# Performance work log

Measured on AMD Instinct MI355X. Metric: run time of the kernel, lower is better.

The kernel has to match this reference:

```python
import jax, jax.numpy as jnp
import numpy as np

N = 62          # EEG channels (nodes per graph)
B = 512         # graphs in batch
K = 2           # SGConv propagation steps
F_IN = 128
H = 64
C = 3


def _complete_graph_edge_index():
    # edge e = g*N*N + i*N + j connects node g*N+i -> g*N+j,
    # matching edge_weight = Wsym.reshape(-1).repeat(B) ordering.
    base = np.arange(N)
    ii = np.tile(np.repeat(base, N), B)
    jj = np.tile(np.tile(base, N), B)
    off = np.repeat(np.arange(B) * N, N * N)
    return jnp.asarray(np.stack([off + ii, off + jj]).astype(np.int32))


def setup_inputs() -> dict:
    key = jax.random.key(0)
    ks = jax.random.split(key, 6)
    n_total = B * N
    x = jax.random.normal(ks[0], (n_total, F_IN), dtype=jnp.float32)
    edge_weight_tril = jax.random.normal(ks[1], (N * (N + 1) // 2,), dtype=jnp.float32)
    W1 = jax.random.normal(ks[2], (H, F_IN), dtype=jnp.float32) * (1.0 / np.sqrt(F_IN))
    b1 = jax.random.normal(ks[3], (H,), dtype=jnp.float32) * 0.01
    W2 = jax.random.normal(ks[4], (C, H), dtype=jnp.float32) * (1.0 / np.sqrt(H))
    b2 = jax.random.normal(ks[5], (C,), dtype=jnp.float32) * 0.01
    edge_index = _complete_graph_edge_index()
    batch = jnp.asarray(np.repeat(np.arange(B), N).astype(np.int32))
    return {"x": x, "edge_weight_tril": edge_weight_tril, "W1": W1, "b1": b1,
            "W2": W2, "b2": b2, "edge_index": edge_index, "batch": batch,
            "batch_size": B}


def reference(x, edge_weight_tril, W1, b1, W2, b2, edge_index, batch, batch_size):
    n_total = x.shape[0]
    # rebuild symmetric dense adjacency from lower-tri params
    xs, ys = np.tril_indices(N)
    Wm = jnp.zeros((N, N), dtype=x.dtype).at[xs, ys].set(edge_weight_tril)
    Wsym = Wm + Wm.T - jnp.diag(jnp.diag(Wm))
    ew = jnp.tile(Wsym.reshape(-1), batch_size)            # [B*N*N]

    row, col = edge_index[0], edge_index[1]
    # symmetric normalization (graph already contains self loops)
    deg = jax.ops.segment_sum(jnp.abs(ew), row, num_segments=n_total)
    dinv = jnp.where(deg > 0, deg ** -0.5, 0.0)
    norm = dinv[row] * ew * dinv[col]                      # [E]

    # K-step SGConv propagation: gather, scale, scatter-add
    h = x
    for _ in range(K):
        h = jax.ops.segment_sum(norm[:, None] * h[row], col, num_segments=n_total)

    h = jax.nn.relu(h @ W1.T + b1)                         # [n_total, H]
    pooled = jax.ops.segment_sum(h, batch, num_segments=batch_size)  # global_add_pool
    latent_v = pooled                                      # dropout in eval mode = identity
    logits = latent_v @ W2.T + b2
    logp = jax.nn.log_softmax(logits, axis=-1)
    return latent_v, logp
```

## Files before the change

### kernel.cpp

```cpp
#include <hip/hip_runtime.h>
#include <math.h>

#define NN  62
#define BGR 512
#define FIN 128
#define HD  64
#define NC  3

typedef __attribute__((ext_vector_type(8))) short          bf16x8;
typedef __attribute__((ext_vector_type(4))) float          f32x4;
typedef __attribute__((ext_vector_type(4))) unsigned short us4;

static __device__ __forceinline__ unsigned short f2bf(float f) {
    union { float f; unsigned u; } v; v.f = f;
    unsigned u = v.u;
    return (unsigned short)((u + 0x7fffu + ((u >> 16) & 1u)) >> 16);
}
static __device__ __forceinline__ float bf2f(unsigned short h) {
    union { unsigned u; float f; } v; v.u = ((unsigned)h) << 16;
    return v.f;
}


__global__ __launch_bounds__(256) void precomp(
    const float* __restrict__ tril, const float* __restrict__ W1,
    unsigned short* __restrict__ ws) {
    __shared__ unsigned short AH[9216];
    __shared__ float dinvS[64];

    const int t = threadIdx.x;
    const int lane = t & 63, wv = t >> 6, quad = lane >> 4, l15 = lane & 15;

    {
        const float4* w14 = (const float4*)W1;
        for (int e = t; e < 2048; e += 256) {
            int h = e >> 5, f4 = e & 31;
            float4 v = w14[e];
            us4 hh, ll;
            hh[0] = f2bf(v.x); ll[0] = f2bf(v.x - bf2f(hh[0]));
            hh[1] = f2bf(v.y); ll[1] = f2bf(v.y - bf2f(hh[1]));
            hh[2] = f2bf(v.z); ll[2] = f2bf(v.z - bf2f(hh[2]));
            hh[3] = f2bf(v.w); ll[3] = f2bf(v.w - bf2f(hh[3]));
            *(us4*)&ws[ 8192 + h * 136 + f4 * 4] = hh;
            *(us4*)&ws[16896 + h * 136 + f4 * 4] = ll;
        }
    }

    if (t < 64) {
        float s = 0.f;
        if (t < NN) {
            for (int j = 0; j < NN; ++j) {
                int hi = max(t, j), lo = min(t, j);
                s += fabsf(tril[hi * (hi + 1) / 2 + lo]);
            }
            s = (s > 0.f) ? (1.0f / sqrtf(s)) : 0.f;
        }
        dinvS[t] = s;
    }
    __syncthreads();

    for (int e4 = t; e4 < 1024; e4 += 256) {
        int i = e4 >> 4, j0 = (e4 & 15) * 4;
        float di = dinvS[i];
        float4 dj4 = *(float4*)&dinvS[j0];
        float dja[4] = {dj4.x, dj4.y, dj4.z, dj4.w};
        us4 hh, ll;
#pragma unroll
        for (int r = 0; r < 4; ++r) {
            int j = j0 + r;
            float w = 0.f;
            if (i < NN && j < NN) {
                int hi = max(i, j), lo = min(i, j);
                w = tril[hi * (hi + 1) / 2 + lo];
            }
            float v = di * w * dja[r];
            hh[r] = f2bf(v);
            ll[r] = f2bf(v - bf2f(hh[r]));
        }
        *(us4*)&AH[       i * 72 + j0] = hh;
        *(us4*)&AH[4608 + i * 72 + j0] = ll;
    }
    __syncthreads();

    f32x4 za0 = {0,0,0,0}, za1 = {0,0,0,0}, za2 = {0,0,0,0}, za3 = {0,0,0,0};
    {
        const int arow = (16 * wv + l15) * 72 + quad * 8;
#pragma unroll
        for (int c = 0; c < 2; ++c) {
            bf16x8 ahi = *(bf16x8*)&AH[arow + c * 32];
            bf16x8 alo = *(bf16x8*)&AH[4608 + arow + c * 32];
#define ATILE(ACC, NT) { \
            int bo = (16 * NT + l15) * 72 + quad * 8 + c * 32; \
            bf16x8 bhi = *(bf16x8*)&AH[bo]; \
            bf16x8 blo = *(bf16x8*)&AH[4608 + bo]; \
            ACC = __builtin_amdgcn_mfma_f32_16x16x32_bf16(ahi, bhi, ACC, 0, 0, 0); \
            ACC = __builtin_amdgcn_mfma_f32_16x16x32_bf16(ahi, blo, ACC, 0, 0, 0); \
            ACC = __builtin_amdgcn_mfma_f32_16x16x32_bf16(alo, bhi, ACC, 0, 0, 0); \
            ACC = __builtin_amdgcn_mfma_f32_16x16x32_bf16(alo, blo, ACC, 0, 0, 0); }
            ATILE(za0, 0) ATILE(za1, 1) ATILE(za2, 2) ATILE(za3, 3)
#undef ATILE
        }
    }

    {
        const int mbase = 16 * wv + quad * 4;
#define A2W(ACC, NT) { \
        int n = 16 * NT + l15; \
        us4 hh, ll; \
        hh[0] = f2bf(ACC[0]); ll[0] = f2bf(ACC[0] - bf2f(hh[0])); \
        hh[1] = f2bf(ACC[1]); ll[1] = f2bf(ACC[1] - bf2f(hh[1])); \
        hh[2] = f2bf(ACC[2]); ll[2] = f2bf(ACC[2] - bf2f(hh[2])); \
        hh[3] = f2bf(ACC[3]); ll[3] = f2bf(ACC[3] - bf2f(hh[3])); \
        *(us4*)&ws[       n * 64 + mbase] = hh; \
        *(us4*)&ws[4096 + n * 64 + mbase] = ll; }
        A2W(za0, 0) A2W(za1, 1) A2W(za2, 2) A2W(za3, 3)
#undef A2W
    }
}

__global__ __launch_bounds__(256) void gcn_all(
    const float* __restrict__ x, const float* __restrict__ b1,
    const float* __restrict__ W2, const float* __restrict__ b2,
    const unsigned short* __restrict__ ws, float* __restrict__ out) {
    __shared__ unsigned short SH[34816];
    __shared__ float TAIL[1088 + 64];
    float* partial = TAIL;
    float* b1S     = TAIL + 1088;

    const int t = threadIdx.x;
    const int g = blockIdx.x;
    const int lane = t & 63, wv = t >> 6, quad = lane >> 4, l15 = lane & 15;

    if (t < 16) *(float4*)&b1S[4 * t] = ((const float4*)b1)[t];

    const int a2off = (16 * wv + l15) * 64 + quad * 8;
    bf16x8 A2h0 = *(const bf16x8*)&ws[a2off];
    bf16x8 A2l0 = *(const bf16x8*)&ws[4096 + a2off];
    bf16x8 A2h1 = *(const bf16x8*)&ws[a2off + 32];
    bf16x8 A2l1 = *(const bf16x8*)&ws[4096 + a2off + 32];

    const float4* xg4 = (const float4*)(x + (size_t)g * NN * FIN);
    for (int e = t; e < 2048; e += 256) {
        int row = e >> 5, k4 = e & 31;
        float4 v = {0.f, 0.f, 0.f, 0.f};
        if (e < 1984) v = xg4[e];
        us4 hh, ll;
        hh[0] = f2bf(v.x); ll[0] = f2bf(v.x - bf2f(hh[0]));
        hh[1] = f2bf(v.y); ll[1] = f2bf(v.y - bf2f(hh[1]));
        hh[2] = f2bf(v.z); ll[2] = f2bf(v.z - bf2f(hh[2]));
        hh[3] = f2bf(v.w); ll[3] = f2bf(v.w - bf2f(hh[3]));
        *(us4*)&SH[       row * 136 + k4 * 4] = hh;
        *(us4*)&SH[8704 + row * 136 + k4 * 4] = ll;
    }
    {
        const uint4* src = (const uint4*)(ws + 8192);
        uint4* dst = (uint4*)(SH + 17408);
        for (int i = t; i < 2176; i += 256) dst[i] = src[i];
    }
    __syncthreads();

    f32x4 y0 = {0,0,0,0}, y1 = {0,0,0,0}, y2 = {0,0,0,0}, y3 = {0,0,0,0};
    {
        const int arow = (16 * wv + l15) * 136 + quad * 8;
#pragma unroll
        for (int c = 0; c < 4; ++c) {
            bf16x8 ahi = *(bf16x8*)&SH[arow + c * 32];
            bf16x8 alo = *(bf16x8*)&SH[8704 + arow + c * 32];
#define P1TILE(ACC, NT) { \
            int bo = (16 * NT + l15) * 136 + quad * 8 + c * 32; \
            bf16x8 bhi = *(bf16x8*)&SH[17408 + bo]; \
            bf16x8 blo = *(bf16x8*)&SH[26112 + bo]; \
            ACC = __builtin_amdgcn_mfma_f32_16x16x32_bf16(ahi, bhi, ACC, 0, 0, 0); \
            ACC = __builtin_amdgcn_mfma_f32_16x16x32_bf16(ahi, blo, ACC, 0, 0, 0); \
            ACC = __builtin_amdgcn_mfma_f32_16x16x32_bf16(alo, bhi, ACC, 0, 0, 0); \
            ACC = __builtin_amdgcn_mfma_f32_16x16x32_bf16(alo, blo, ACC, 0, 0, 0); }
            P1TILE(y0, 0) P1TILE(y1, 1) P1TILE(y2, 2) P1TILE(y3, 3)
#undef P1TILE
        }
    }
    __syncthreads();

    {
        const int mbase = 16 * wv + quad * 4;
#define SPLITW(ACC, NT) { \
        int n = 16 * NT + l15; \
        us4 hh, ll; \
        hh[0] = f2bf(ACC[0]); ll[0] = f2bf(ACC[0] - bf2f(hh[0])); \
        hh[1] = f2bf(ACC[1]); ll[1] = f2bf(ACC[1] - bf2f(hh[1])); \
        hh[2] = f2bf(ACC[2]); ll[2] = f2bf(ACC[2] - bf2f(hh[2])); \
        hh[3] = f2bf(ACC[3]); ll[3] = f2bf(ACC[3] - bf2f(hh[3])); \
        *(us4*)&SH[       n * 72 + mbase] = hh; \
        *(us4*)&SH[4608 + n * 72 + mbase] = ll; }
        SPLITW(y0, 0) SPLITW(y1, 1) SPLITW(y2, 2) SPLITW(y3, 3)
#undef SPLITW
    }
    __syncthreads();

    f32x4 z0 = {0,0,0,0}, z1 = {0,0,0,0}, z2 = {0,0,0,0}, z3 = {0,0,0,0};
    {
#define P2TILE(ACC, NT, AH_, AL_, CO) { \
        int bo = (16 * NT + l15) * 72 + quad * 8 + CO; \
        bf16x8 bhi = *(bf16x8*)&SH[bo]; \
        bf16x8 blo = *(bf16x8*)&SH[4608 + bo]; \
        ACC = __builtin_amdgcn_mfma_f32_16x16x32_bf16(AH_, bhi, ACC, 0, 0, 0); \
        ACC = __builtin_amdgcn_mfma_f32_16x16x32_bf16(AH_, blo, ACC, 0, 0, 0); \
        ACC = __builtin_amdgcn_mfma_f32_16x16x32_bf16(AL_, bhi, ACC, 0, 0, 0); \
        ACC = __builtin_amdgcn_mfma_f32_16x16x32_bf16(AL_, blo, ACC, 0, 0, 0); }
        P2TILE(z0, 0, A2h0, A2l0, 0) P2TILE(z1, 1, A2h0, A2l0, 0)
        P2TILE(z2, 2, A2h0, A2l0, 0) P2TILE(z3, 3, A2h0, A2l0, 0)
        P2TILE(z0, 0, A2h1, A2l1, 32) P2TILE(z1, 1, A2h1, A2l1, 32)
        P2TILE(z2, 2, A2h1, A2l1, 32) P2TILE(z3, 3, A2h1, A2l1, 32)
#undef P2TILE
    }

    {
        const int mbase = 16 * wv + quad * 4;
        const int slot = 4 * wv + quad;
#define POOL(ACC, NT) { \
        int n = 16 * NT + l15; \
        float bn = b1S[n]; \
        float p = 0.f; \
        if (mbase + 0 < 62) p += fmaxf(ACC[0] + bn, 0.f); \
        if (mbase + 1 < 62) p += fmaxf(ACC[1] + bn, 0.f); \
        if (mbase + 2 < 62) p += fmaxf(ACC[2] + bn, 0.f); \
        if (mbase + 3 < 62) p += fmaxf(ACC[3] + bn, 0.f); \
        partial[n * 17 + slot] = p; }
        POOL(z0, 0) POOL(z1, 1) POOL(z2, 2) POOL(z3, 3)
#undef POOL
    }
    __syncthreads();

    if (t < HD) {
        float s = 0.f;
#pragma unroll
        for (int q = 0; q < 16; ++q) s += partial[t * 17 + q];
        out[(size_t)g * HD + t] = s;
        float l0 = s * W2[t];
        float l1 = s * W2[64 + t];
        float l2 = s * W2[128 + t];
#pragma unroll
        for (int off = 32; off > 0; off >>= 1) {
            l0 += __shfl_down(l0, off);
            l1 += __shfl_down(l1, off);
            l2 += __shfl_down(l2, off);
        }
        if (t == 0) {
            l0 += b2[0]; l1 += b2[1]; l2 += b2[2];
            float m = fmaxf(l0, fmaxf(l1, l2));
            float lse = m + logf(expf(l0 - m) + expf(l1 - m) + expf(l2 - m));
            float* lp = out + (size_t)BGR * HD + (size_t)g * NC;
            lp[0] = l0 - lse; lp[1] = l1 - lse; lp[2] = l2 - lse;
        }
    }
}

extern "C" void kernel_launch(void* const* d_in, const int* in_sizes, int n_in,
                              void* d_out, int out_size, void* d_ws, size_t ws_size,
                              hipStream_t stream) {
    const float* x    = (const float*)d_in[0];
    const float* tril = (const float*)d_in[1];
    const float* W1   = (const float*)d_in[2];
    const float* b1   = (const float*)d_in[3];
    const float* W2   = (const float*)d_in[4];
    const float* b2   = (const float*)d_in[5];
    float* out = (float*)d_out;
    unsigned short* ws = (unsigned short*)d_ws;

    precomp<<<1, 256, 0, stream>>>(tril, W1, ws);
    gcn_all<<<BGR, 256, 0, stream>>>(x, b1, W2, b2, ws, out);
}
```

Baseline: 105.1 us.

## Fuse adjacency precompute into main kernel and drop lo*lo split-bf16 MFMA terms

Removes the single-block precomp launch. Every block now recomputes dinv, the normalized A, A^2 and the bf16 hi/lo split of W1 itself, and reads x rows straight into registers instead of staging them in LDS. It also drops the lo*lo MFMA term in all three matmuls, cutting MFMA count by a quarter at a small precision cost. The trade is redundant per-block A^2 and W1 conversion work and heavier register use, in exchange for removing the serial launch dependency and the LDS staging of x.

```diff
diff --git a/kernel.cpp b/kernel.cpp
--- a/kernel.cpp
+++ b/kernel.cpp
@@ -21,28 +21,44 @@
     return v.f;
 }
 
-
-__global__ __launch_bounds__(256) void precomp(
-    const float* __restrict__ tril, const float* __restrict__ W1,
-    unsigned short* __restrict__ ws) {
-    __shared__ unsigned short AH[9216];
-    __shared__ float dinvS[64];
+__global__ __launch_bounds__(256) void gcn_all(
+    const float* __restrict__ x, const float* __restrict__ tril,
+    const float* __restrict__ W1, const float* __restrict__ b1,
+    const float* __restrict__ W2, const float* __restrict__ b2,
+    float* __restrict__ out) {
+    __shared__ unsigned short SH[35840];
+    __shared__ float TAIL[1088 + 64 + 64];
+    float* partial = TAIL;
+    float* b1S     = TAIL + 1088;
+    float* dinvS   = TAIL + 1152;
 
     const int t = threadIdx.x;
+    const int g = blockIdx.x;
     const int lane = t & 63, wv = t >> 6, quad = lane >> 4, l15 = lane & 15;
 
-    {
-        const float4* w14 = (const float4*)W1;
-        for (int e = t; e < 2048; e += 256) {
-            int h = e >> 5, f4 = e & 31;
-            float4 v = w14[e];
-            us4 hh, ll;
-            hh[0] = f2bf(v.x); ll[0] = f2bf(v.x - bf2f(hh[0]));
-            hh[1] = f2bf(v.y); ll[1] = f2bf(v.y - bf2f(hh[1]));
-            hh[2] = f2bf(v.z); ll[2] = f2bf(v.z - bf2f(hh[2]));
-            hh[3] = f2bf(v.w); ll[3] = f2bf(v.w - bf2f(hh[3]));
-            *(us4*)&ws[ 8192 + h * 136 + f4 * 4] = hh;
-            *(us4*)&ws[16896 + h * 136 + f4 * 4] = ll;
+    if (t < 16) *(float4*)&b1S[4 * t] = ((const float4*)b1)[t];
+
+    bf16x8 xh[4], xl[4];
+    {
+        const int xr = 16 * wv + l15;
+        if (xr < NN) {
+            const float* xrow = x + (size_t)g * NN * FIN + (size_t)xr * FIN + quad * 8;
+#pragma unroll
+            for (int c = 0; c < 4; ++c) {
+                float4 a = *(const float4*)(xrow + c * 32);
+                float4 b = *(const float4*)(xrow + c * 32 + 4);
+                float vv[8] = {a.x, a.y, a.z, a.w, b.x, b.y, b.z, b.w};
+#pragma unroll
+                for (int k = 0; k < 8; ++k) {
+                    unsigned short h = f2bf(vv[k]);
+                    xh[c][k] = (short)h;
+                    xl[c][k] = (short)f2bf(vv[k] - bf2f(h));
+                }
+            }
+        } else {
+            bf16x8 zv = {0, 0, 0, 0, 0, 0, 0, 0};
+#pragma unroll
+            for (int c = 0; c < 4; ++c) { xh[c] = zv; xl[c] = zv; }
         }
     }
 
@@ -77,140 +93,99 @@
             hh[r] = f2bf(v);
             ll[r] = f2bf(v - bf2f(hh[r]));
         }
-        *(us4*)&AH[       i * 72 + j0] = hh;
-        *(us4*)&AH[4608 + i * 72 + j0] = ll;
+        *(us4*)&SH[17408 + i * 72 + j0] = hh;
+        *(us4*)&SH[22016 + i * 72 + j0] = ll;
+    }
+    {
+        const float4* w14 = (const float4*)W1;
+        for (int e = t; e < 2048; e += 256) {
+            int h = e >> 5, f4 = e & 31;
+            float4 v = w14[e];
+            us4 hh, ll;
+            hh[0] = f2bf(v.x); ll[0] = f2bf(v.x - bf2f(hh[0]));
+            hh[1] = f2bf(v.y); ll[1] = f2bf(v.y - bf2f(hh[1]));
+            hh[2] = f2bf(v.z); ll[2] = f2bf(v.z - bf2f(hh[2]));
+            hh[3] = f2bf(v.w); ll[3] = f2bf(v.w - bf2f(hh[3]));
+            *(us4*)&SH[       h * 136 + f4 * 4] = hh;
+            *(us4*)&SH[8704 + h * 136 + f4 * 4] = ll;
+        }
     }
     __syncthreads();
 
     f32x4 za0 = {0,0,0,0}, za1 = {0,0,0,0}, za2 = {0,0,0,0}, za3 = {0,0,0,0};
     {
-        const int arow = (16 * wv + l15) * 72 + quad * 8;
+        const int arow = 17408 + (16 * wv + l15) * 72 + quad * 8;
 #pragma unroll
         for (int c = 0; c < 2; ++c) {
-            bf16x8 ahi = *(bf16x8*)&AH[arow + c * 32];
-            bf16x8 alo = *(bf16x8*)&AH[4608 + arow + c * 32];
+            bf16x8 ahi = *(bf16x8*)&SH[arow + c * 32];
+            bf16x8 alo = *(bf16x8*)&SH[4608 + arow + c * 32];
 #define ATILE(ACC, NT) { \
-            int bo = (16 * NT + l15) * 72 + quad * 8 + c * 32; \
-            bf16x8 bhi = *(bf16x8*)&AH[bo]; \
-            bf16x8 blo = *(bf16x8*)&AH[4608 + bo]; \
+            int bo = 17408 + (16 * NT + l15) * 72 + quad * 8 + c * 32; \
+            bf16x8 bhi = *(bf16x8*)&SH[bo]; \
+            bf16x8 blo = *(bf16x8*)&SH[4608 + bo]; \
             ACC = __builtin_amdgcn_mfma_f32_16x16x32_bf16(ahi, bhi, ACC, 0, 0, 0); \
             ACC = __builtin_amdgcn_mfma_f32_16x16x32_bf16(ahi, blo, ACC, 0, 0, 0); \
-            ACC = __builtin_amdgcn_mfma_f32_16x16x32_bf16(alo, bhi, ACC, 0, 0, 0); \
-            ACC = __builtin_amdgcn_mfma_f32_16x16x32_bf16(alo, blo, ACC, 0, 0, 0); }
+            ACC = __builtin_amdgcn_mfma_f32_16x16x32_bf16(alo, bhi, ACC, 0, 0, 0); }
             ATILE(za0, 0) ATILE(za1, 1) ATILE(za2, 2) ATILE(za3, 3)
 #undef ATILE
         }
     }
 
+    f32x4 y0 = {0,0,0,0}, y1 = {0,0,0,0}, y2 = {0,0,0,0}, y3 = {0,0,0,0};
+    {
+#pragma unroll
+        for (int c = 0; c < 4; ++c) {
+            bf16x8 ahi = xh[c];
+            bf16x8 alo = xl[c];
+#define P1TILE(ACC, NT) { \
+            int bo = (16 * NT + l15) * 136 + quad * 8 + c * 32; \
+            bf16x8 bhi = *(bf16x8*)&SH[bo]; \
+            bf16x8 blo = *(bf16x8*)&SH[8704 + bo]; \
+            ACC = __builtin_amdgcn_mfma_f32_16x16x32_bf16(ahi, bhi, ACC, 0, 0, 0); \
+            ACC = __builtin_amdgcn_mfma_f32_16x16x32_bf16(ahi, blo, ACC, 0, 0, 0); \
+            ACC = __builtin_amdgcn_mfma_f32_16x16x32_bf16(alo, bhi, ACC, 0, 0, 0); }
+            P1TILE(y0, 0) P1TILE(y1, 1) P1TILE(y2, 2) P1TILE(y3, 3)
+#undef P1TILE
+        }
+    }
+    __syncthreads();
+
     {
         const int mbase = 16 * wv + quad * 4;
-#define A2W(ACC, NT) { \
+#define SPLITW(ACC, NT, HIOFF, LOOFF) { \
         int n = 16 * NT + l15; \
         us4 hh, ll; \
         hh[0] = f2bf(ACC[0]); ll[0] = f2bf(ACC[0] - bf2f(hh[0])); \
         hh[1] = f2bf(ACC[1]); ll[1] = f2bf(ACC[1] - bf2f(hh[1])); \
         hh[2] = f2bf(ACC[2]); ll[2] = f2bf(ACC[2] - bf2f(hh[2])); \
         hh[3] = f2bf(ACC[3]); ll[3] = f2bf(ACC[3] - bf2f(hh[3])); \
-        *(us4*)&ws[       n * 64 + mbase] = hh; \
-        *(us4*)&ws[4096 + n * 64 + mbase] = ll; }
-        A2W(za0, 0) A2W(za1, 1) A2W(za2, 2) A2W(za3, 3)
-#undef A2W
-    }
-}
-
-__global__ __launch_bounds__(256) void gcn_all(
-    const float* __restrict__ x, const float* __restrict__ b1,
-    const float* __restrict__ W2, const float* __restrict__ b2,
-    const unsigned short* __restrict__ ws, float* __restrict__ out) {
-    __shared__ unsigned short SH[34816];
-    __shared__ float TAIL[1088 + 64];
-    float* partial = TAIL;
-    float* b1S     = TAIL + 1088;
-
-    const int t = threadIdx.x;
-    const int g = blockIdx.x;
-    const int lane = t & 63, wv = t >> 6, quad = lane >> 4, l15 = lane & 15;
-
-    if (t < 16) *(float4*)&b1S[4 * t] = ((const float4*)b1)[t];
-
-    const int a2off = (16 * wv + l15) * 64 + quad * 8;
-    bf16x8 A2h0 = *(const bf16x8*)&ws[a2off];
-    bf16x8 A2l0 = *(const bf16x8*)&ws[4096 + a2off];
-    bf16x8 A2h1 = *(const bf16x8*)&ws[a2off + 32];
-    bf16x8 A2l1 = *(const bf16x8*)&ws[4096 + a2off + 32];
-
-    const float4* xg4 = (const float4*)(x + (size_t)g * NN * FIN);
-    for (int e = t; e < 2048; e += 256) {
-        int row = e >> 5, k4 = e & 31;
-        float4 v = {0.f, 0.f, 0.f, 0.f};
-        if (e < 1984) v = xg4[e];
-        us4 hh, ll;
-        hh[0] = f2bf(v.x); ll[0] = f2bf(v.x - bf2f(hh[0]));
-        hh[1] = f2bf(v.y); ll[1] = f2bf(v.y - bf2f(hh[1]));
-        hh[2] = f2bf(v.z); ll[2] = f2bf(v.z - bf2f(hh[2]));
-        hh[3] = f2bf(v.w); ll[3] = f2bf(v.w - bf2f(hh[3]));
-        *(us4*)&SH[       row * 136 + k4 * 4] = hh;
-        *(us4*)&SH[8704 + row * 136 + k4 * 4] = ll;
-    }
-    {
-        const uint4* src = (const uint4*)(ws + 8192);
-        uint4* dst = (uint4*)(SH + 17408);
-        for (int i = t; i < 2176; i += 256) dst[i] = src[i];
-    }
-    __syncthreads();
-
-    f32x4 y0 = {0,0,0,0}, y1 = {0,0,0,0}, y2 = {0,0,0,0}, y3 = {0,0,0,0};
-    {
-        const int arow = (16 * wv + l15) * 136 + quad * 8;
-#pragma unroll
-        for (int c = 0; c < 4; ++c) {
+        *(us4*)&SH[(HIOFF) + n * 72 + mbase] = hh; \
+        *(us4*)&SH[(LOOFF) + n * 72 + mbase] = ll; }
+        SPLITW(y0, 0, 26624, 31232) SPLITW(y1, 1, 26624, 31232)
+        SPLITW(y2, 2, 26624, 31232) SPLITW(y3, 3, 26624, 31232)
+        SPLITW(za0, 0, 17408, 22016) SPLITW(za1, 1, 17408, 22016)
+        SPLITW(za2, 2, 17408, 22016) SPLITW(za3, 3, 17408, 22016)
+#undef SPLITW
+    }
+    __syncthreads();
+
+    f32x4 z0 = {0,0,0,0}, z1 = {0,0,0,0}, z2 = {0,0,0,0}, z3 = {0,0,0,0};
+    {
+        const int arow = 17408 + (16 * wv + l15) * 72 + quad * 8;
+#pragma unroll
+        for (int c = 0; c < 2; ++c) {
             bf16x8 ahi = *(bf16x8*)&SH[arow + c * 32];
-            bf16x8 alo = *(bf16x8*)&SH[8704 + arow + c * 32];
-#define P1TILE(ACC, NT) { \
-            int bo = (16 * NT + l15) * 136 + quad * 8 + c * 32; \
-            bf16x8 bhi = *(bf16x8*)&SH[17408 + bo]; \
-            bf16x8 blo = *(bf16x8*)&SH[26112 + bo]; \
+            bf16x8 alo = *(bf16x8*)&SH[4608 + arow + c * 32];
+#define P2TILE(ACC, NT) { \
+            int bo = 26624 + (16 * NT + l15) * 72 + quad * 8 + c * 32; \
+            bf16x8 bhi = *(bf16x8*)&SH[bo]; \
+            bf16x8 blo = *(bf16x8*)&SH[4608 + bo]; \
             ACC = __builtin_amdgcn_mfma_f32_16x16x32_bf16(ahi, bhi, ACC, 0, 0, 0); \
             ACC = __builtin_amdgcn_mfma_f32_16x16x32_bf16(ahi, blo, ACC, 0, 0, 0); \
-            ACC = __builtin_amdgcn_mfma_f32_16x16x32_bf16(alo, bhi, ACC, 0, 0, 0); \
-            ACC = __builtin_amdgcn_mfma_f32_16x16x32_bf16(alo, blo, ACC, 0, 0, 0); }
-            P1TILE(y0, 0) P1TILE(y1, 1) P1TILE(y2, 2) P1TILE(y3, 3)
-#undef P1TILE
-        }
-    }
-    __syncthreads();
-
-    {
-        const int mbase = 16 * wv + quad * 4;
-#define SPLITW(ACC, NT) { \
-        int n = 16 * NT + l15; \
-        us4 hh, ll; \
-        hh[0] = f2bf(ACC[0]); ll[0] = f2bf(ACC[0] - bf2f(hh[0])); \
-        hh[1] = f2bf(ACC[1]); ll[1] = f2bf(ACC[1] - bf2f(hh[1])); \
-        hh[2] = f2bf(ACC[2]); ll[2] = f2bf(ACC[2] - bf2f(hh[2])); \
-        hh[3] = f2bf(ACC[3]); ll[3] = f2bf(ACC[3] - bf2f(hh[3])); \
-        *(us4*)&SH[       n * 72 + mbase] = hh; \
-        *(us4*)&SH[4608 + n * 72 + mbase] = ll; }
-        SPLITW(y0, 0) SPLITW(y1, 1) SPLITW(y2, 2) SPLITW(y3, 3)
-#undef SPLITW
-    }
-    __syncthreads();
-
-    f32x4 z0 = {0,0,0,0}, z1 = {0,0,0,0}, z2 = {0,0,0,0}, z3 = {0,0,0,0};
-    {
-#define P2TILE(ACC, NT, AH_, AL_, CO) { \
-        int bo = (16 * NT + l15) * 72 + quad * 8 + CO; \
-        bf16x8 bhi = *(bf16x8*)&SH[bo]; \
-        bf16x8 blo = *(bf16x8*)&SH[4608 + bo]; \
-        ACC = __builtin_amdgcn_mfma_f32_16x16x32_bf16(AH_, bhi, ACC, 0, 0, 0); \
-        ACC = __builtin_amdgcn_mfma_f32_16x16x32_bf16(AH_, blo, ACC, 0, 0, 0); \
-        ACC = __builtin_amdgcn_mfma_f32_16x16x32_bf16(AL_, bhi, ACC, 0, 0, 0); \
-        ACC = __builtin_amdgcn_mfma_f32_16x16x32_bf16(AL_, blo, ACC, 0, 0, 0); }
-        P2TILE(z0, 0, A2h0, A2l0, 0) P2TILE(z1, 1, A2h0, A2l0, 0)
-        P2TILE(z2, 2, A2h0, A2l0, 0) P2TILE(z3, 3, A2h0, A2l0, 0)
-        P2TILE(z0, 0, A2h1, A2l1, 32) P2TILE(z1, 1, A2h1, A2l1, 32)
-        P2TILE(z2, 2, A2h1, A2l1, 32) P2TILE(z3, 3, A2h1, A2l1, 32)
+            ACC = __builtin_amdgcn_mfma_f32_16x16x32_bf16(alo, bhi, ACC, 0, 0, 0); }
+            P2TILE(z0, 0) P2TILE(z1, 1) P2TILE(z2, 2) P2TILE(z3, 3)
 #undef P2TILE
+        }
     }
 
     {
@@ -264,8 +239,6 @@
     const float* W2   = (const float*)d_in[4];
     const float* b2   = (const float*)d_in[5];
     float* out = (float*)d_out;
-    unsigned short* ws = (unsigned short*)d_ws;
-
-    precomp<<<1, 256, 0, stream>>>(tril, W1, ws);
-    gcn_all<<<BGR, 256, 0, stream>>>(x, b1, W2, b2, ws, out);
-}
+
+    gcn_all<<<BGR, 256, 0, stream>>>(x, tril, W1, b1, W2, b2, out);
+}
```

Result: faster. 100.7 us (-4.3%).
